# Kernel optimization log

Hardware: AMD Instinct MI355X
Metric: run time of the kernel (lower is better)

## Reference

```python
import jax, jax.numpy as jnp
import numpy as np

N, E, H = 2000, 4096, 256

def setup_inputs() -> dict:
    key = jax.random.key(0)
    ks = jax.random.split(key, 24)
    def rn(k, shape, scale=0.05):
        return jax.random.normal(k, shape, dtype=jnp.float32) * scale
    inp = {
        'x': jax.random.randint(ks[0], (N, 1), 0, 5),
        'pos': rn(ks[1], (N, 3), 1.0),
        'edge_index': jax.random.randint(ks[2], (2, E), 0, N),
        'edge_atr': rn(ks[3], (E, 5), 1.0),
        'emb_table': rn(ks[4], (5, 5), 1.0),
        'lin0_W': rn(ks[5], (H, 8)), 'lin0_b': jnp.zeros((H,), jnp.float32),
        'mlp1_W': rn(ks[6], (128, 5)), 'mlp1_b': jnp.zeros((128,), jnp.float32),
        'mlp2_W': rn(ks[7], (H * H, 128), 0.01), 'mlp2_b': jnp.zeros((H * H,), jnp.float32),
        'conv_b': jnp.zeros((H,), jnp.float32),
        'gru_Wih': rn(ks[8], (3 * H, H)), 'gru_Whh': rn(ks[9], (3 * H, H)),
        'gru_bih': jnp.zeros((3 * H,), jnp.float32), 'gru_bhh': jnp.zeros((3 * H,), jnp.float32),
        'lin1_W': rn(ks[10], (H, 2 * H)), 'lin1_b': jnp.zeros((H,), jnp.float32),
        'lin2_W': rn(ks[11], (242, H)), 'lin2_b': jnp.zeros((242,), jnp.float32),
        'l6_W1': rn(ks[12], (128, 2 * H)), 'l6_b1': jnp.zeros((128,), jnp.float32),
        'bn_g': jnp.ones((128,), jnp.float32), 'bn_b': jnp.zeros((128,), jnp.float32),
        'l6_W2': rn(ks[13], (1, 128)), 'l6_b2': jnp.zeros((1,), jnp.float32),
    }
    return inp

def _gru_step(m, h, Wih, Whh, bih, bhh):
    gi = m @ Wih.T + bih  # [N,3H]
    gh = h @ Whh.T + bhh
    gir, giz, gin = jnp.split(gi, 3, axis=1)
    ghr, ghz, ghn = jnp.split(gh, 3, axis=1)
    r = jax.nn.sigmoid(gir + ghr)
    z = jax.nn.sigmoid(giz + ghz)
    n = jnp.tanh(gin + r * ghn)
    return (1.0 - z) * n + z * h

def reference(x, pos, edge_index, edge_atr, emb_table, lin0_W, lin0_b,
              mlp1_W, mlp1_b, mlp2_W, mlp2_b, conv_b,
              gru_Wih, gru_Whh, gru_bih, gru_bhh,
              lin1_W, lin1_b, lin2_W, lin2_b,
              l6_W1, l6_b1, bn_g, bn_b, l6_W2, l6_b2):
    node_emb = emb_table[x[:, 0]]                      # [N,5]
    in_p = jnp.concatenate([node_emb, pos], axis=1)    # [N,8]
    out = jax.nn.relu(in_p @ lin0_W.T + lin0_b)        # [N,H]
    h = out
    row, col = edge_index[0], edge_index[1]
    # edge-conditioned weights (edge_atr is loop-invariant -> compute once)
    he = jax.nn.relu(edge_atr @ mlp1_W.T + mlp1_b)     # [E,128]
    W_e = (he @ mlp2_W.T + mlp2_b).reshape(E, H, H)    # [E,H,H]
    counts = jnp.clip(jax.ops.segment_sum(jnp.ones((E,), jnp.float32), col, num_segments=N), 1.0)
    for _ in range(3):
        msg = jnp.einsum('eh,eho->eo', out[row], W_e)  # gather + per-edge matmul
        agg = jax.ops.segment_sum(msg, col, num_segments=N) / counts[:, None] + conv_b
        m = jax.nn.relu(agg)
        h = _gru_step(m, h, gru_Wih, gru_Whh, gru_bih, gru_bhh)
        out = h
    out_concat = jnp.concatenate([out[row], out[col]], axis=1)  # [E,2H]
    o1 = jax.nn.relu(out_concat @ lin1_W.T + lin1_b)
    out2 = o1 @ lin2_W.T + lin2_b                       # [E,242]
    # lin6: Linear -> BatchNorm1d (batch stats, training mode) -> ReLU -> Linear
    h1 = out_concat @ l6_W1.T + l6_b1                   # [E,128]
    mu = jnp.mean(h1, axis=0)
    var = jnp.var(h1, axis=0)
    h1n = (h1 - mu) * jax.lax.rsqrt(var + 1e-5) * bn_g + bn_b
    precs = jax.nn.relu(h1n) @ l6_W2.T + l6_b2          # [E,1]
    return (out2, precs)
```

## Files before the change

kernel.cpp:

```cpp
#include <hip/hip_runtime.h>
#include <hip/hip_bf16.h>

constexpr int N_ = 2000;
constexpr int E_ = 4096;
constexpr int H_ = 256;
constexpr int KH_ = 128;
constexpr int NV_ = H_ * KH_;
constexpr int MPAD_ = 2048;
constexpr int NG_ = 768;
constexpr float VSCALE = 64.f;
constexpr float VSCALE_INV = 1.f / 64.f;

typedef short bf16x8 __attribute__((ext_vector_type(8)));
typedef float f32x4  __attribute__((ext_vector_type(4)));
typedef float f32x2  __attribute__((ext_vector_type(2)));

__device__ __forceinline__ float bf_lo(unsigned u) { return __uint_as_float(u << 16); }
__device__ __forceinline__ float bf_hi(unsigned u) { return __uint_as_float(u & 0xffff0000u); }
__device__ __forceinline__ short bfbits(float f) {
    __hip_bfloat16 b = __float2bfloat16(f);
    return *(short*)&b;
}

#define PIPE_WAIT_ENTER(N_OUTST)                                   \
    asm volatile("s_waitcnt vmcnt(" #N_OUTST ")" ::: "memory");    \
    __builtin_amdgcn_s_barrier();                                  \
    asm volatile("" ::: "memory");                                 \
    __builtin_amdgcn_sched_barrier(0);

#define PIPE_EXIT()                                                \
    __builtin_amdgcn_sched_barrier(0);                             \
    asm volatile("" ::: "memory");                                 \
    __builtin_amdgcn_s_barrier();

__global__ void k_lin0(const int* __restrict__ x, const float* __restrict__ pos,
                       const float* __restrict__ emb, const float* __restrict__ W,
                       const float* __restrict__ b, float* __restrict__ out,
                       __hip_bfloat16* __restrict__ Abf) {
    int n = blockIdx.x, t = threadIdx.x;
    if (n >= N_) { Abf[(size_t)n * H_ + t] = __float2bfloat16(0.f); return; }
    __shared__ float in_p[8];
    if (t < 5) in_p[t] = emb[x[n] * 5 + t];
    else if (t < 8) in_p[t] = pos[n * 3 + (t - 5)];
    __syncthreads();
    float acc = b[t];
#pragma unroll
    for (int i = 0; i < 8; i++) acc += in_p[i] * W[t * 8 + i];
    float v = fmaxf(acc, 0.f);
    out[n * H_ + t] = v;
    Abf[(size_t)n * H_ + t] = __float2bfloat16(v);
}

__global__ void k_he(const float* __restrict__ ea, const float* __restrict__ W,
                     const float* __restrict__ b, float* __restrict__ he) {
    int e = blockIdx.x, t = threadIdx.x;
    __shared__ float a[5];
    if (t < 5) a[t] = ea[e * 5 + t];
    __syncthreads();
    float acc = b[t];
#pragma unroll
    for (int i = 0; i < 5; i++) acc += a[i] * W[t * 5 + i];
    he[e * KH_ + t] = fmaxf(acc, 0.f);
}

__global__ void k_counts(const int* __restrict__ ei, float* __restrict__ counts) {
    int e = blockIdx.x * blockDim.x + threadIdx.x;
    if (e < E_) atomicAdd(&counts[ei[E_ + e]], 1.0f);
}

__global__ void k_trans_bt(const float* __restrict__ W, __hip_bfloat16* __restrict__ Bt) {
    __shared__ float tile[32][68];
    int t = threadIdx.x;
    int n0 = blockIdx.x * 64, k0 = blockIdx.y * 32;
#pragma unroll
    for (int i = 0; i < 2; i++) {
        int idx = t + i * 256;
        int kk = idx >> 4, nn = (idx & 15) * 4;
        float4 f = *(const float4*)&W[(size_t)(k0 + kk) * NV_ + n0 + nn];
        *(float4*)&tile[kk][nn] = f;
    }
    __syncthreads();
#pragma unroll
    for (int i = 0; i < 2; i++) {
        int idx = t + i * 256;
        int nn = idx >> 3, k4 = (idx & 7) * 4;
        short4 s;
        s.x = bfbits(tile[k4 + 0][nn]);
        s.y = bfbits(tile[k4 + 1][nn]);
        s.z = bfbits(tile[k4 + 2][nn]);
        s.w = bfbits(tile[k4 + 3][nn]);
        *(short4*)&Bt[(size_t)(n0 + nn) * H_ + k0 + k4] = s;
    }
}

__global__ void k_prep_w(const float* __restrict__ Wih, const float* __restrict__ Whh,
                         const float* __restrict__ lin1W, const float* __restrict__ l6W1,
                         const float* __restrict__ lin2W, const float* __restrict__ b2,
                         __hip_bfloat16* __restrict__ WihB, __hip_bfloat16* __restrict__ WhhB,
                         __hip_bfloat16* __restrict__ Bpk,
                         __hip_bfloat16* __restrict__ lin2Wb, __hip_bfloat16* __restrict__ BtB) {
    int i = blockIdx.x * 256 + threadIdx.x;
    if (i < NG_ * H_) {
        WihB[i] = __float2bfloat16(Wih[i]);
        WhhB[i] = __float2bfloat16(Whh[i]);
    }
    Bpk[i] = __float2bfloat16(i < 256 * 512 ? lin1W[i] : l6W1[i - 256 * 512]);
    if (i < 128 * 2 * H_) {
        int r = i >> 8, k = i & 255;
        lin2Wb[i] = __float2bfloat16(r < 242 ? lin2W[r * H_ + k] : 0.f);
        int o = i >> 8, h = i & 255;
        BtB[o * H_ + h] = __float2bfloat16(b2[h * H_ + o]);
    }
}

__global__ void k_concat(const int* __restrict__ ei, const float* __restrict__ h,
                         __hip_bfloat16* __restrict__ Cbf) {
    int e = blockIdx.x, t = threadIdx.x;
    int r = ei[e], c = ei[E_ + e];
    Cbf[(size_t)e * 512 + t]       = __float2bfloat16(h[(size_t)r * H_ + t]);
    Cbf[(size_t)e * 512 + 256 + t] = __float2bfloat16(h[(size_t)c * H_ + t]);
}

template <int KD, bool RELU, bool OUT_BF16>
__global__ __launch_bounds__(256, 3) void k_gemm_nt(const __hip_bfloat16* __restrict__ A,
                                                    const __hip_bfloat16* __restrict__ Bt,
                                                    float* __restrict__ Cf,
                                                    __hip_bfloat16* __restrict__ Cb,
                                                    const float* __restrict__ bias,
                                                    int ldc, int ncols, int mvalid) {
    __shared__ __align__(16) short As[2][4096];
    __shared__ __align__(16) short Bs[2][4096];
    int t = threadIdx.x;
    int lane = t & 63, wave = t >> 6;
    int wm = wave >> 1, wn = wave & 1;
    int quad = lane >> 4, l16 = lane & 15;
    int row0 = blockIdx.y * 128, col0 = blockIdx.x * 128;

    f32x4 acc[4][4] = {};
    int r_ld = (lane >> 2);
    int koff = (((lane & 3) ^ ((lane >> 3) & 3)) * 8);
    int swz = (l16 >> 1) & 3;
    constexpr int NST = KD / 32;

    auto stage = [&](int buf, int k0) {
#pragma unroll
        for (int c = 0; c < 4; c++) {
            int q = wave * 4 + c;
            int ch = q & 7;
            int r = ch * 16 + r_ld;
            const __hip_bfloat16* gp;
            short* lp;
            if (q < 8) { gp = A  + (size_t)(row0 + r) * KD + k0 + koff; lp = &As[buf][ch * 512]; }
            else       { gp = Bt + (size_t)(col0 + r) * KD + k0 + koff; lp = &Bs[buf][ch * 512]; }
            __builtin_amdgcn_global_load_lds(
                (const __attribute__((address_space(1))) unsigned int*)(uintptr_t)gp,
                (__attribute__((address_space(3))) unsigned int*)(uintptr_t)lp,
                16, 0, 0);
        }
    };

    stage(0, 0);
    for (int kk = 0; kk < NST; kk++) {
        int cur = kk & 1;
        if (kk + 1 < NST) {
            stage(cur ^ 1, (kk + 1) * 32);
            PIPE_WAIT_ENTER(4)
        } else {
            PIPE_WAIT_ENTER(0)
        }
        bf16x8 a[4], b[4];
#pragma unroll
        for (int i = 0; i < 4; i++)
            a[i] = *(const bf16x8*)&As[cur][(wm * 64 + i * 16 + l16) * 32 + ((quad ^ swz) << 3)];
#pragma unroll
        for (int j = 0; j < 4; j++)
            b[j] = *(const bf16x8*)&Bs[cur][(wn * 64 + j * 16 + l16) * 32 + ((quad ^ swz) << 3)];
#pragma unroll
        for (int i = 0; i < 4; i++)
#pragma unroll
            for (int j = 0; j < 4; j++)
                acc[i][j] = __builtin_amdgcn_mfma_f32_16x16x32_bf16(a[i], b[j], acc[i][j], 0, 0, 0);
        PIPE_EXIT()
    }

#pragma unroll
    for (int i = 0; i < 4; i++) {
        int gm0 = row0 + wm * 64 + i * 16 + quad * 4;
#pragma unroll
        for (int r = 0; r < 4; r++) {
            int gm = gm0 + r;
            if (gm < mvalid) {
#pragma unroll
                for (int j = 0; j < 4; j++) {
                    int col = col0 + wn * 64 + l16 + j * 16;
                    if (col < ncols) {
                        float v = acc[i][j][r];
                        if (bias) v += bias[col];
                        if (RELU) v = fmaxf(v, 0.f);
                        if (OUT_BF16) Cb[(size_t)gm * ldc + col] = __float2bfloat16(v);
                        else          Cf[(size_t)gm * ldc + col] = v;
                    }
                }
            }
        }
    }
}

__global__ __launch_bounds__(256, 4) void k_gemm_VP(const __hip_bfloat16* __restrict__ Abf,
                                                    const __hip_bfloat16* __restrict__ Bt,
                                                    const __hip_bfloat16* __restrict__ WhhB,
                                                    const __hip_bfloat16* __restrict__ BtB,
                                                    const float* __restrict__ bhh,
                                                    float* __restrict__ gh,
                                                    float* __restrict__ outb,
                                                    unsigned char* __restrict__ V8) {
    __shared__ __align__(16) short As[2][4096];
    __shared__ __align__(16) short Bs[2][4096];
    int bid = blockIdx.x;
    int t = threadIdx.x;
    int lane = t & 63, wave = t >> 6;
    int wm = wave >> 1, wn = wave & 1;
    int quad = lane >> 4, l16 = lane & 15;
    int r_ld = (lane >> 2);
    int koff = (((lane & 3) ^ ((lane >> 3) & 3)) * 8);
    int swz = (l16 >> 1) & 3;

    if (bid < 128) {
        int pbx = bid & 7, pby = bid >> 3;
        bool ob = (pbx >= 6);
        const __hip_bfloat16* Bp = ob ? BtB : WhhB;
        int col0 = ob ? (pbx - 6) * 128 : pbx * 128;
        int ldc = ob ? H_ : NG_;
        float* C = ob ? outb : gh;
        int row0 = pby * 128;

        f32x4 acc[4][4] = {};
        auto stage = [&](int buf, int k0) {
#pragma unroll
            for (int c = 0; c < 4; c++) {
                int q = wave * 4 + c;
                int ch = q & 7;
                int r = ch * 16 + r_ld;
                const __hip_bfloat16* gp;
                short* lp;
                if (q < 8) { gp = Abf + ((size_t)(row0 + r) << 8) + k0 + koff; lp = &As[buf][ch * 512]; }
                else       { gp = Bp  + ((size_t)(col0 + r) << 8) + k0 + koff; lp = &Bs[buf][ch * 512]; }
                __builtin_amdgcn_global_load_lds(
                    (const __attribute__((address_space(1))) unsigned int*)(uintptr_t)gp,
                    (__attribute__((address_space(3))) unsigned int*)(uintptr_t)lp,
                    16, 0, 0);
            }
        };
        stage(0, 0);
        for (int kk = 0; kk < 8; kk++) {
            int cur = kk & 1;
            if (kk + 1 < 8) {
                stage(cur ^ 1, (kk + 1) * 32);
                PIPE_WAIT_ENTER(4)
            } else {
                PIPE_WAIT_ENTER(0)
            }
            bf16x8 a[4], b[4];
#pragma unroll
            for (int i = 0; i < 4; i++)
                a[i] = *(const bf16x8*)&As[cur][(wm * 64 + i * 16 + l16) * 32 + ((quad ^ swz) << 3)];
#pragma unroll
            for (int j = 0; j < 4; j++)
                b[j] = *(const bf16x8*)&Bs[cur][(wn * 64 + j * 16 + l16) * 32 + ((quad ^ swz) << 3)];
#pragma unroll
            for (int i = 0; i < 4; i++)
#pragma unroll
                for (int j = 0; j < 4; j++)
                    acc[i][j] = __builtin_amdgcn_mfma_f32_16x16x32_bf16(a[i], b[j], acc[i][j], 0, 0, 0);
            PIPE_EXIT()
        }
#pragma unroll
        for (int i = 0; i < 4; i++) {
            int gm0 = row0 + wm * 64 + i * 16 + quad * 4;
#pragma unroll
            for (int r = 0; r < 4; r++) {
                int gm = gm0 + r;
                if (gm < N_) {
#pragma unroll
                    for (int j = 0; j < 4; j++) {
                        int col = col0 + wn * 64 + l16 + j * 16;
                        float v = acc[i][j][r] + (ob ? 0.f : bhh[col]);
                        C[(size_t)gm * ldc + col] = v;
                    }
                }
            }
        }
        return;
    }

    int vb = bid - 128;
    int bx = vb & 255, by = vb >> 8;
    int row0 = by * 128, col0 = bx * 128;
    int obase = bx * 8;
    int kb = (bx >> 5) * 16;
    short* Ps = &As[0][0];

    f32x4 acc[4][4] = {};
    auto stage = [&](int buf, int k0) {
#pragma unroll
        for (int c = 0; c < 4; c++) {
            int q = wave * 4 + c;
            int ch = q & 7;
            const __hip_bfloat16* gp;
            short* lp;
            if (q < 8) {
                gp = Abf + ((size_t)(row0 + ch * 16 + r_ld) << 8) + k0 + koff;
                lp = &As[buf][ch * 512];
            } else {
                int nv = ((obase + ch) & 255) * 128 + kb + r_ld;
                gp = Bt + ((size_t)nv << 8) + k0 + koff;
                lp = &Bs[buf][ch * 512];
            }
            __builtin_amdgcn_global_load_lds(
                (const __attribute__((address_space(1))) unsigned int*)(uintptr_t)gp,
                (__attribute__((address_space(3))) unsigned int*)(uintptr_t)lp,
                16, 0, 0);
        }
    };
    stage(0, 0);
    for (int kk = 0; kk < 8; kk++) {
        int cur = kk & 1;
        if (kk + 1 < 8) {
            stage(cur ^ 1, (kk + 1) * 32);
            PIPE_WAIT_ENTER(4)
        } else {
            PIPE_WAIT_ENTER(0)
        }
        bf16x8 a[4], b[4];
#pragma unroll
        for (int i = 0; i < 4; i++)
            a[i] = *(const bf16x8*)&As[cur][(wm * 64 + i * 16 + l16) * 32 + ((quad ^ swz) << 3)];
#pragma unroll
        for (int j = 0; j < 4; j++)
            b[j] = *(const bf16x8*)&Bs[cur][(wn * 64 + j * 16 + l16) * 32 + ((quad ^ swz) << 3)];
#pragma unroll
        for (int i = 0; i < 4; i++)
#pragma unroll
            for (int j = 0; j < 4; j++)
                acc[i][j] = __builtin_amdgcn_mfma_f32_16x16x32_bf16(a[i], b[j], acc[i][j], 0, 0, 0);
        PIPE_EXIT()
    }

#pragma unroll
    for (int pp = 0; pp < 4; pp++) {
        if (wm == (pp >> 1)) {
#pragma unroll
            for (int ii = 0; ii < 2; ii++) {
                const int i = (pp & 1) * 2 + ii;
                int lr = ii * 16 + quad * 4;
#pragma unroll
                for (int r = 0; r < 4; r++) {
#pragma unroll
                    for (int j = 0; j < 4; j++) {
                        int col = wn * 64 + j * 16 + l16;
                        Ps[(lr + r) * 136 + col] = bfbits(acc[i][j][r] * VSCALE);
                    }
                }
            }
        }
        __syncthreads();
        {
            int row = t >> 3;
            int col = (t & 7) * 16;
            int gm = row0 + pp * 32 + row;
            if (gm < N_) {
                uint4 ua = *(const uint4*)&Ps[row * 136 + col];
                uint4 ub = *(const uint4*)&Ps[row * 136 + col + 8];
                unsigned p0 = __builtin_amdgcn_cvt_pk_fp8_f32(bf_lo(ua.x), bf_hi(ua.x), 0, false);
                p0 = __builtin_amdgcn_cvt_pk_fp8_f32(bf_lo(ua.y), bf_hi(ua.y), p0, true);
                unsigned p1 = __builtin_amdgcn_cvt_pk_fp8_f32(bf_lo(ua.z), bf_hi(ua.z), 0, false);
                p1 = __builtin_amdgcn_cvt_pk_fp8_f32(bf_lo(ua.w), bf_hi(ua.w), p1, true);
                unsigned p2 = __builtin_amdgcn_cvt_pk_fp8_f32(bf_lo(ub.x), bf_hi(ub.x), 0, false);
                p2 = __builtin_amdgcn_cvt_pk_fp8_f32(bf_lo(ub.y), bf_hi(ub.y), p2, true);
                unsigned p3 = __builtin_amdgcn_cvt_pk_fp8_f32(bf_lo(ub.z), bf_hi(ub.z), 0, false);
                p3 = __builtin_amdgcn_cvt_pk_fp8_f32(bf_lo(ub.w), bf_hi(ub.w), p3, true);
                uint4 o4;
                o4.x = p0; o4.y = p1; o4.z = p2; o4.w = p3;
                *(uint4*)(V8 + (size_t)gm * NV_ + col0 + col) = o4;
            }
        }
        __syncthreads();
    }
}

__global__ __launch_bounds__(256, 3) void k_gemm_tail(const __hip_bfloat16* __restrict__ A,
                                                      const __hip_bfloat16* __restrict__ Bpk,
                                                      const float* __restrict__ b1,
                                                      const float* __restrict__ b2,
                                                      __hip_bfloat16* __restrict__ o1bf,
                                                      float* __restrict__ h1) {
    __shared__ __align__(16) short As[2][4096];
    __shared__ __align__(16) short Bs[2][4096];
    int t = threadIdx.x;
    int lane = t & 63, wave = t >> 6;
    int wm = wave >> 1, wn = wave & 1;
    int quad = lane >> 4, l16 = lane & 15;
    int row0 = blockIdx.y * 128, col0 = blockIdx.x * 128;

    f32x4 acc[4][4] = {};
    int r_ld = (lane >> 2);
    int koff = (((lane & 3) ^ ((lane >> 3) & 3)) * 8);
    int swz = (l16 >> 1) & 3;

    auto stage = [&](int buf, int k0) {
#pragma unroll
        for (int c = 0; c < 4; c++) {
            int q = wave * 4 + c;
            int ch = q & 7;
            int r = ch * 16 + r_ld;
            const __hip_bfloat16* gp;
            short* lp;
            if (q < 8) { gp = A   + (size_t)(row0 + r) * 512 + k0 + koff; lp = &As[buf][ch * 512]; }
            else       { gp = Bpk + (size_t)(col0 + r) * 512 + k0 + koff; lp = &Bs[buf][ch * 512]; }
            __builtin_amdgcn_global_load_lds(
                (const __attribute__((address_space(1))) unsigned int*)(uintptr_t)gp,
                (__attribute__((address_space(3))) unsigned int*)(uintptr_t)lp,
                16, 0, 0);
        }
    };

    stage(0, 0);
    for (int kk = 0; kk < 16; kk++) {
        int cur = kk & 1;
        if (kk + 1 < 16) {
            stage(cur ^ 1, (kk + 1) * 32);
            PIPE_WAIT_ENTER(4)
        } else {
            PIPE_WAIT_ENTER(0)
        }
        bf16x8 a[4], b[4];
#pragma unroll
        for (int i = 0; i < 4; i++)
            a[i] = *(const bf16x8*)&As[cur][(wm * 64 + i * 16 + l16) * 32 + ((quad ^ swz) << 3)];
#pragma unroll
        for (int j = 0; j < 4; j++)
            b[j] = *(const bf16x8*)&Bs[cur][(wn * 64 + j * 16 + l16) * 32 + ((quad ^ swz) << 3)];
#pragma unroll
        for (int i = 0; i < 4; i++)
#pragma unroll
            for (int j = 0; j < 4; j++)
                acc[i][j] = __builtin_amdgcn_mfma_f32_16x16x32_bf16(a[i], b[j], acc[i][j], 0, 0, 0);
        PIPE_EXIT()
    }

#pragma unroll
    for (int i = 0; i < 4; i++) {
        int gm0 = row0 + wm * 64 + i * 16 + quad * 4;
#pragma unroll
        for (int r = 0; r < 4; r++) {
            int gm = gm0 + r;
#pragma unroll
            for (int j = 0; j < 4; j++) {
                int col = col0 + wn * 64 + l16 + j * 16;
                float v = acc[i][j][r];
                if (col < 256) {
                    v = fmaxf(v + b1[col], 0.f);
                    o1bf[(size_t)gm * H_ + col] = __float2bfloat16(v);
                } else {
                    h1[(size_t)gm * 128 + (col - 256)] = v + b2[col - 256];
                }
            }
        }
    }
}

__global__ void k_msg(const int* __restrict__ ei, const float* __restrict__ he,
                      const unsigned char* __restrict__ V8, const float* __restrict__ outb,
                      float* __restrict__ agg) {
    int e = blockIdx.x, o = threadIdx.x;
    __shared__ float hs[KH_];
    if (o < KH_) hs[o] = he[e * KH_ + o] * VSCALE_INV;
    __syncthreads();
    int r = ei[e], c = ei[E_ + e];
    float acc = outb[(size_t)r * H_ + o];
    const unsigned char* vbase = V8 + (size_t)r * NV_ + o * 16;
#pragma unroll
    for (int q = 0; q < 8; q++) {
        uint4 u = *(const uint4*)(vbase + (size_t)q * 4096);
        const float* hp = hs + q * 16;
        f32x2 f;
        f = __builtin_amdgcn_cvt_pk_f32_fp8(u.x, false); acc += hp[0]  * f.x + hp[1]  * f.y;
        f = __builtin_amdgcn_cvt_pk_f32_fp8(u.x, true);  acc += hp[2]  * f.x + hp[3]  * f.y;
        f = __builtin_amdgcn_cvt_pk_f32_fp8(u.y, false); acc += hp[4]  * f.x + hp[5]  * f.y;
        f = __builtin_amdgcn_cvt_pk_f32_fp8(u.y, true);  acc += hp[6]  * f.x + hp[7]  * f.y;
        f = __builtin_amdgcn_cvt_pk_f32_fp8(u.z, false); acc += hp[8]  * f.x + hp[9]  * f.y;
        f = __builtin_amdgcn_cvt_pk_f32_fp8(u.z, true);  acc += hp[10] * f.x + hp[11] * f.y;
        f = __builtin_amdgcn_cvt_pk_f32_fp8(u.w, false); acc += hp[12] * f.x + hp[13] * f.y;
        f = __builtin_amdgcn_cvt_pk_f32_fp8(u.w, true);  acc += hp[14] * f.x + hp[15] * f.y;
    }
    atomicAdd(&agg[(size_t)c * H_ + o], acc);
}

__global__ void k_m(float* __restrict__ agg, const float* __restrict__ counts,
                    const float* __restrict__ conv_b, __hip_bfloat16* __restrict__ Mbf) {
    int i = blockIdx.x * blockDim.x + threadIdx.x;
    if (i >= N_ * H_) return;
    int n = i >> 8, o = i & 255;
    float c = fmaxf(counts[n], 1.0f);
    float a = agg[i];
    agg[i] = 0.f;
    Mbf[i] = __float2bfloat16(fmaxf(a / c + conv_b[o], 0.f));
}

__global__ void k_gru_update(const float* __restrict__ gi, const float* __restrict__ gh,
                             float* __restrict__ h, __hip_bfloat16* __restrict__ Abf) {
    int i = blockIdx.x * blockDim.x + threadIdx.x;
    if (i >= N_ * H_) return;
    int n = i >> 8, j = i & 255;
    const float* gip = gi + (size_t)n * NG_;
    const float* ghp = gh + (size_t)n * NG_;
    float r = 1.f / (1.f + expf(-(gip[j] + ghp[j])));
    float z = 1.f / (1.f + expf(-(gip[H_ + j] + ghp[H_ + j])));
    float nn = tanhf(gip[2 * H_ + j] + r * ghp[2 * H_ + j]);
    float hv = (1.f - z) * nn + z * h[i];
    h[i] = hv;
    Abf[i] = __float2bfloat16(hv);
}

__global__ void k_bnstats(const float* __restrict__ h1, float* __restrict__ mu,
                          float* __restrict__ rsig) {
    int j = blockIdx.x, t = threadIdx.x;
    float s = 0.f, ss = 0.f;
    for (int e = t; e < E_; e += 256) {
        float v = h1[(size_t)e * 128 + j];
        s += v;
        ss += v * v;
    }
    __shared__ float rs[256], rss[256];
    rs[t] = s; rss[t] = ss;
    __syncthreads();
    for (int off = 128; off > 0; off >>= 1) {
        if (t < off) { rs[t] += rs[t + off]; rss[t] += rss[t + off]; }
        __syncthreads();
    }
    if (t == 0) {
        float m_ = rs[0] / E_;
        float v_ = rss[0] / E_ - m_ * m_;
        mu[j] = m_;
        rsig[j] = rsqrtf(v_ + 1e-5f);
    }
}

__global__ void k_precs(const float* __restrict__ h1, const float* __restrict__ mu,
                        const float* __restrict__ rsig, const float* __restrict__ g,
                        const float* __restrict__ bb, const float* __restrict__ W2,
                        const float* __restrict__ b2, float* __restrict__ out) {
    int e = blockIdx.x * blockDim.x + threadIdx.x;
    if (e >= E_) return;
    float acc = b2[0];
#pragma unroll 4
    for (int j = 0; j < 128; j++) {
        float v = (h1[(size_t)e * 128 + j] - mu[j]) * rsig[j] * g[j] + bb[j];
        acc += fmaxf(v, 0.f) * W2[j];
    }
    out[(size_t)E_ * 242 + e] = acc;
}

extern "C" void kernel_launch(void* const* d_in, const int* in_sizes, int n_in,
                              void* d_out, int out_size, void* d_ws, size_t ws_size,
                              hipStream_t stream) {
    const int*   x        = (const int*)  d_in[0];
    const float* pos      = (const float*)d_in[1];
    const int*   ei       = (const int*)  d_in[2];
    const float* edge_atr = (const float*)d_in[3];
    const float* emb      = (const float*)d_in[4];
    const float* lin0_W   = (const float*)d_in[5];
    const float* lin0_b   = (const float*)d_in[6];
    const float* mlp1_W   = (const float*)d_in[7];
    const float* mlp1_b   = (const float*)d_in[8];
    const float* mlp2_W   = (const float*)d_in[9];
    const float* mlp2_b   = (const float*)d_in[10];
    const float* conv_b   = (const float*)d_in[11];
    const float* gru_Wih  = (const float*)d_in[12];
    const float* gru_Whh  = (const float*)d_in[13];
    const float* gru_bih  = (const float*)d_in[14];
    const float* gru_bhh  = (const float*)d_in[15];
    const float* lin1_W   = (const float*)d_in[16];
    const float* lin1_b   = (const float*)d_in[17];
    const float* lin2_W   = (const float*)d_in[18];
    const float* lin2_b   = (const float*)d_in[19];
    const float* l6_W1    = (const float*)d_in[20];
    const float* l6_b1    = (const float*)d_in[21];
    const float* bn_g     = (const float*)d_in[22];
    const float* bn_b     = (const float*)d_in[23];
    const float* l6_W2    = (const float*)d_in[24];
    const float* l6_b2    = (const float*)d_in[25];
    float* out = (float*)d_out;

    char* w = (char*)d_ws;
    size_t off = 0;
    auto alloc = [&](size_t bytes) -> void* {
        void* p = w + off;
        off = (off + bytes + 255) & ~(size_t)255;
        return p;
    };
    float* hbuf   = (float*)alloc((size_t)N_ * H_ * 4);
    float* aggm   = (float*)alloc((size_t)N_ * H_ * 4);
    float* outb   = (float*)alloc((size_t)N_ * H_ * 4);
    float* he     = (float*)alloc((size_t)E_ * KH_ * 4);
    float* gi     = (float*)alloc((size_t)N_ * NG_ * 4);
    float* gh     = (float*)alloc((size_t)N_ * NG_ * 4);
    float* h1     = (float*)alloc((size_t)E_ * 128 * 4);
    float* counts = (float*)alloc((size_t)N_ * 4);
    float* mu     = (float*)alloc(128 * 4);
    float* rsig   = (float*)alloc(128 * 4);
    unsigned char* V8      = (unsigned char*)alloc((size_t)N_ * NV_);
    __hip_bfloat16* Abf    = (__hip_bfloat16*)alloc((size_t)MPAD_ * H_ * 2);
    __hip_bfloat16* Mbf    = (__hip_bfloat16*)alloc((size_t)MPAD_ * H_ * 2);
    __hip_bfloat16* Bt     = (__hip_bfloat16*)alloc((size_t)NV_ * H_ * 2);
    __hip_bfloat16* WihB   = (__hip_bfloat16*)alloc((size_t)NG_ * H_ * 2);
    __hip_bfloat16* WhhB   = (__hip_bfloat16*)alloc((size_t)NG_ * H_ * 2);
    __hip_bfloat16* Bpk    = (__hip_bfloat16*)alloc((size_t)384 * 512 * 2);
    __hip_bfloat16* lin2Wb = (__hip_bfloat16*)alloc((size_t)H_ * H_ * 2);
    __hip_bfloat16* BtB    = (__hip_bfloat16*)alloc((size_t)H_ * H_ * 2);
    __hip_bfloat16* Cbf    = (__hip_bfloat16*)alloc((size_t)E_ * 2 * H_ * 2);
    __hip_bfloat16* o1bf   = (__hip_bfloat16*)alloc((size_t)E_ * H_ * 2);

    k_lin0<<<MPAD_, 256, 0, stream>>>(x, pos, emb, lin0_W, lin0_b, hbuf, Abf);
    k_he<<<E_, 128, 0, stream>>>(edge_atr, mlp1_W, mlp1_b, he);
    hipMemsetAsync(counts, 0, (size_t)N_ * 4, stream);
    hipMemsetAsync(aggm, 0, (size_t)N_ * H_ * 4, stream);
    k_counts<<<(E_ + 255) / 256, 256, 0, stream>>>(ei, counts);
    k_trans_bt<<<dim3(NV_ / 64, H_ / 32), 256, 0, stream>>>(mlp2_W, Bt);
    k_prep_w<<<768, 256, 0, stream>>>(gru_Wih, gru_Whh, lin1_W, l6_W1, lin2_W, mlp2_b,
                                      WihB, WhhB, Bpk, lin2Wb, BtB);

    for (int it = 0; it < 3; it++) {
        k_gemm_VP<<<128 + (NV_ / 128) * (MPAD_ / 128), 256, 0, stream>>>(
            Abf, Bt, WhhB, BtB, gru_bhh, gh, outb, V8);
        k_msg<<<E_, 256, 0, stream>>>(ei, he, V8, outb, aggm);
        k_m<<<(N_ * H_ + 255) / 256, 256, 0, stream>>>(aggm, counts, conv_b, Mbf);
        k_gemm_nt<256, false, false><<<dim3(6, MPAD_ / 128), 256, 0, stream>>>(
            Mbf, WihB, gi, nullptr, gru_bih, NG_, NG_, N_);
        k_gru_update<<<(N_ * H_ + 255) / 256, 256, 0, stream>>>(gi, gh, hbuf, Abf);
    }

    k_concat<<<E_, 256, 0, stream>>>(ei, hbuf, Cbf);
    k_gemm_tail<<<dim3(3, E_ / 128), 256, 0, stream>>>(Cbf, Bpk, lin1_b, l6_b1, o1bf, h1);
    k_gemm_nt<256, false, false><<<dim3(2, E_ / 128), 256, 0, stream>>>(
        o1bf, lin2Wb, out, nullptr, lin2_b, 242, 242, E_);
    k_bnstats<<<128, 256, 0, stream>>>(h1, mu, rsig);
    k_precs<<<(E_ + 255) / 256, 256, 0, stream>>>(h1, mu, rsig, bn_g, bn_b, l6_W2, l6_b2, out);
}
```

Before: 458.9 us.

## Fuse mean/relu prologue into GI GEMM and gather-concat into tail GEMM

The separate k_m kernel, which normalized, biased and relu'd the aggregate into bf16, is folded into a new GEMM that reads fp32 aggregates directly and transforms them in registers before writing to LDS. Likewise the concat gather kernel is folded into the tail GEMM, which gathers node rows by edge index. Aggregate zeroing moves into the GRU update. This removes several launches and intermediate buffers per iteration. In exchange, half the waves now do register-staged loads and conversion instead of async global-to-LDS copies, which may weaken the load pipelining.

```diff
diff --git a/kernel.cpp b/kernel.cpp
--- a/kernel.cpp
+++ b/kernel.cpp
@@ -111,14 +111,6 @@
         int o = i >> 8, h = i & 255;
         BtB[o * H_ + h] = __float2bfloat16(b2[h * H_ + o]);
     }
-}
-
-__global__ void k_concat(const int* __restrict__ ei, const float* __restrict__ h,
-                         __hip_bfloat16* __restrict__ Cbf) {
-    int e = blockIdx.x, t = threadIdx.x;
-    int r = ei[e], c = ei[E_ + e];
-    Cbf[(size_t)e * 512 + t]       = __float2bfloat16(h[(size_t)r * H_ + t]);
-    Cbf[(size_t)e * 512 + 256 + t] = __float2bfloat16(h[(size_t)c * H_ + t]);
 }
 
 template <int KD, bool RELU, bool OUT_BF16>
@@ -388,12 +380,140 @@
     }
 }
 
-__global__ __launch_bounds__(256, 3) void k_gemm_tail(const __hip_bfloat16* __restrict__ A,
-                                                      const __hip_bfloat16* __restrict__ Bpk,
-                                                      const float* __restrict__ b1,
-                                                      const float* __restrict__ b2,
-                                                      __hip_bfloat16* __restrict__ o1bf,
-                                                      float* __restrict__ h1) {
+__global__ __launch_bounds__(256, 3) void k_gemm_gi(const float* __restrict__ agg,
+                                                    const float* __restrict__ counts,
+                                                    const float* __restrict__ conv_b,
+                                                    const __hip_bfloat16* __restrict__ WihB,
+                                                    const float* __restrict__ bih,
+                                                    float* __restrict__ gi) {
+    __shared__ __align__(16) short As[2][4096];
+    __shared__ __align__(16) short Bs[2][4096];
+    __shared__ __align__(16) float conv_lds[256];
+    int t = threadIdx.x;
+    int lane = t & 63, wave = t >> 6;
+    int wm = wave >> 1, wn = wave & 1;
+    int quad = lane >> 4, l16 = lane & 15;
+    int row0 = blockIdx.y * 128, col0 = blockIdx.x * 128;
+    int r_ld = (lane >> 2);
+    int koff = (((lane & 3) ^ ((lane >> 3) & 3)) * 8);
+    int swz = (l16 >> 1) & 3;
+    bool arole = (wave < 2);
+
+    conv_lds[t] = conv_b[t];
+    __syncthreads();
+
+    f32x4 acc[4][4] = {};
+    float rcv[4];
+    const float* asrc[4];
+    if (arole) {
+#pragma unroll
+        for (int c = 0; c < 4; c++) {
+            int ch = wave * 4 + c;
+            int row = row0 + ch * 16 + r_ld;
+            int rowc = row < N_ ? row : N_ - 1;
+            rcv[c] = 1.f / fmaxf(counts[rowc], 1.f);
+            asrc[c] = agg + (size_t)rowc * 256;
+        }
+    }
+    float4 R[2][4][2];
+
+    auto loadA = [&](int buf, int k0) {
+#pragma unroll
+        for (int c = 0; c < 4; c++) {
+            R[buf][c][0] = *(const float4*)(asrc[c] + k0 + koff);
+            R[buf][c][1] = *(const float4*)(asrc[c] + k0 + koff + 4);
+        }
+    };
+    auto stageB = [&](int buf, int k0) {
+#pragma unroll
+        for (int c = 0; c < 4; c++) {
+            int ch = (wave * 4 + c) & 7;
+            const __hip_bfloat16* gp = WihB + (size_t)(col0 + ch * 16 + r_ld) * 256 + k0 + koff;
+            short* lp = &Bs[buf][ch * 512];
+            __builtin_amdgcn_global_load_lds(
+                (const __attribute__((address_space(1))) unsigned int*)(uintptr_t)gp,
+                (__attribute__((address_space(3))) unsigned int*)(uintptr_t)lp,
+                16, 0, 0);
+        }
+    };
+    auto writeA = [&](int buf, int k0) {
+        float4 cb0 = *(const float4*)&conv_lds[k0 + koff];
+        float4 cb1 = *(const float4*)&conv_lds[k0 + koff + 4];
+#pragma unroll
+        for (int c = 0; c < 4; c++) {
+            int ch = wave * 4 + c;
+            float rc = rcv[c];
+            float4 a0 = R[buf][c][0], a1 = R[buf][c][1];
+            bf16x8 v;
+            v[0] = bfbits(fmaxf(a0.x * rc + cb0.x, 0.f));
+            v[1] = bfbits(fmaxf(a0.y * rc + cb0.y, 0.f));
+            v[2] = bfbits(fmaxf(a0.z * rc + cb0.z, 0.f));
+            v[3] = bfbits(fmaxf(a0.w * rc + cb0.w, 0.f));
+            v[4] = bfbits(fmaxf(a1.x * rc + cb1.x, 0.f));
+            v[5] = bfbits(fmaxf(a1.y * rc + cb1.y, 0.f));
+            v[6] = bfbits(fmaxf(a1.z * rc + cb1.z, 0.f));
+            v[7] = bfbits(fmaxf(a1.w * rc + cb1.w, 0.f));
+            *(bf16x8*)&As[buf][ch * 512 + lane * 8] = v;
+        }
+    };
+
+    if (arole) loadA(0, 0); else stageB(0, 0);
+#pragma unroll
+    for (int kk = 0; kk < 8; kk++) {
+        const int cur = kk & 1;
+        if (kk + 1 < 8) {
+            if (arole) loadA(cur ^ 1, (kk + 1) * 32);
+            else       stageB(cur ^ 1, (kk + 1) * 32);
+        }
+        if (arole) {
+            writeA(cur, kk * 32);
+            asm volatile("s_waitcnt lgkmcnt(0)" ::: "memory");
+        } else {
+            if (kk + 1 < 8) { asm volatile("s_waitcnt vmcnt(4)" ::: "memory"); }
+            else            { asm volatile("s_waitcnt vmcnt(0)" ::: "memory"); }
+        }
+        __builtin_amdgcn_s_barrier();
+        asm volatile("" ::: "memory");
+        __builtin_amdgcn_sched_barrier(0);
+        bf16x8 a[4], b[4];
+#pragma unroll
+        for (int i = 0; i < 4; i++)
+            a[i] = *(const bf16x8*)&As[cur][(wm * 64 + i * 16 + l16) * 32 + ((quad ^ swz) << 3)];
+#pragma unroll
+        for (int j = 0; j < 4; j++)
+            b[j] = *(const bf16x8*)&Bs[cur][(wn * 64 + j * 16 + l16) * 32 + ((quad ^ swz) << 3)];
+#pragma unroll
+        for (int i = 0; i < 4; i++)
+#pragma unroll
+            for (int j = 0; j < 4; j++)
+                acc[i][j] = __builtin_amdgcn_mfma_f32_16x16x32_bf16(a[i], b[j], acc[i][j], 0, 0, 0);
+        PIPE_EXIT()
+    }
+
+#pragma unroll
+    for (int i = 0; i < 4; i++) {
+        int gm0 = row0 + wm * 64 + i * 16 + quad * 4;
+#pragma unroll
+        for (int r = 0; r < 4; r++) {
+            int gm = gm0 + r;
+            if (gm < N_) {
+#pragma unroll
+                for (int j = 0; j < 4; j++) {
+                    int col = col0 + wn * 64 + l16 + j * 16;
+                    gi[(size_t)gm * NG_ + col] = acc[i][j][r] + bih[col];
+                }
+            }
+        }
+    }
+}
+
+__global__ __launch_bounds__(256, 3) void k_gemm_tail2(const int* __restrict__ ei,
+                                                       const float* __restrict__ h,
+                                                       const __hip_bfloat16* __restrict__ Bpk,
+                                                       const float* __restrict__ b1,
+                                                       const float* __restrict__ b2,
+                                                       __hip_bfloat16* __restrict__ o1bf,
+                                                       float* __restrict__ h1) {
     __shared__ __align__(16) short As[2][4096];
     __shared__ __align__(16) short Bs[2][4096];
     int t = threadIdx.x;
@@ -401,38 +521,77 @@
     int wm = wave >> 1, wn = wave & 1;
     int quad = lane >> 4, l16 = lane & 15;
     int row0 = blockIdx.y * 128, col0 = blockIdx.x * 128;
-
-    f32x4 acc[4][4] = {};
     int r_ld = (lane >> 2);
     int koff = (((lane & 3) ^ ((lane >> 3) & 3)) * 8);
     int swz = (l16 >> 1) & 3;
-
-    auto stage = [&](int buf, int k0) {
-#pragma unroll
-        for (int c = 0; c < 4; c++) {
-            int q = wave * 4 + c;
-            int ch = q & 7;
-            int r = ch * 16 + r_ld;
-            const __hip_bfloat16* gp;
-            short* lp;
-            if (q < 8) { gp = A   + (size_t)(row0 + r) * 512 + k0 + koff; lp = &As[buf][ch * 512]; }
-            else       { gp = Bpk + (size_t)(col0 + r) * 512 + k0 + koff; lp = &Bs[buf][ch * 512]; }
+    bool arole = (wave < 2);
+
+    f32x4 acc[4][4] = {};
+    const float* src0[4];
+    const float* src1[4];
+    if (arole) {
+#pragma unroll
+        for (int c = 0; c < 4; c++) {
+            int ch = wave * 4 + c;
+            int e = row0 + ch * 16 + r_ld;
+            src0[c] = h + (size_t)ei[e] * 256;
+            src1[c] = h + (size_t)ei[E_ + e] * 256;
+        }
+    }
+    float4 R[2][4][2];
+
+    auto loadA = [&](int buf, int k0) {
+        bool hi = (k0 >= 256);
+        int kc = (k0 & 255) + koff;
+#pragma unroll
+        for (int c = 0; c < 4; c++) {
+            const float* s = hi ? src1[c] : src0[c];
+            R[buf][c][0] = *(const float4*)(s + kc);
+            R[buf][c][1] = *(const float4*)(s + kc + 4);
+        }
+    };
+    auto stageB = [&](int buf, int k0) {
+#pragma unroll
+        for (int c = 0; c < 4; c++) {
+            int ch = (wave * 4 + c) & 7;
+            const __hip_bfloat16* gp = Bpk + (size_t)(col0 + ch * 16 + r_ld) * 512 + k0 + koff;
+            short* lp = &Bs[buf][ch * 512];
             __builtin_amdgcn_global_load_lds(
                 (const __attribute__((address_space(1))) unsigned int*)(uintptr_t)gp,
                 (__attribute__((address_space(3))) unsigned int*)(uintptr_t)lp,
                 16, 0, 0);
         }
     };
-
-    stage(0, 0);
+    auto writeA = [&](int buf) {
+#pragma unroll
+        for (int c = 0; c < 4; c++) {
+            int ch = wave * 4 + c;
+            float4 a0 = R[buf][c][0], a1 = R[buf][c][1];
+            bf16x8 v;
+            v[0] = bfbits(a0.x); v[1] = bfbits(a0.y); v[2] = bfbits(a0.z); v[3] = bfbits(a0.w);
+            v[4] = bfbits(a1.x); v[5] = bfbits(a1.y); v[6] = bfbits(a1.z); v[7] = bfbits(a1.w);
+            *(bf16x8*)&As[buf][ch * 512 + lane * 8] = v;
+        }
+    };
+
+    if (arole) loadA(0, 0); else stageB(0, 0);
+#pragma unroll
     for (int kk = 0; kk < 16; kk++) {
-        int cur = kk & 1;
+        const int cur = kk & 1;
         if (kk + 1 < 16) {
-            stage(cur ^ 1, (kk + 1) * 32);
-            PIPE_WAIT_ENTER(4)
+            if (arole) loadA(cur ^ 1, (kk + 1) * 32);
+            else       stageB(cur ^ 1, (kk + 1) * 32);
+        }
+        if (arole) {
+            writeA(cur);
+            asm volatile("s_waitcnt lgkmcnt(0)" ::: "memory");
         } else {
-            PIPE_WAIT_ENTER(0)
-        }
+            if (kk + 1 < 16) { asm volatile("s_waitcnt vmcnt(4)" ::: "memory"); }
+            else             { asm volatile("s_waitcnt vmcnt(0)" ::: "memory"); }
+        }
+        __builtin_amdgcn_s_barrier();
+        asm volatile("" ::: "memory");
+        __builtin_amdgcn_sched_barrier(0);
         bf16x8 a[4], b[4];
 #pragma unroll
         for (int i = 0; i < 4; i++)
@@ -496,19 +655,9 @@
     atomicAdd(&agg[(size_t)c * H_ + o], acc);
 }
 
-__global__ void k_m(float* __restrict__ agg, const float* __restrict__ counts,
-                    const float* __restrict__ conv_b, __hip_bfloat16* __restrict__ Mbf) {
-    int i = blockIdx.x * blockDim.x + threadIdx.x;
-    if (i >= N_ * H_) return;
-    int n = i >> 8, o = i & 255;
-    float c = fmaxf(counts[n], 1.0f);
-    float a = agg[i];
-    agg[i] = 0.f;
-    Mbf[i] = __float2bfloat16(fmaxf(a / c + conv_b[o], 0.f));
-}
-
 __global__ void k_gru_update(const float* __restrict__ gi, const float* __restrict__ gh,
-                             float* __restrict__ h, __hip_bfloat16* __restrict__ Abf) {
+                             float* __restrict__ h, __hip_bfloat16* __restrict__ Abf,
+                             float* __restrict__ agg) {
     int i = blockIdx.x * blockDim.x + threadIdx.x;
     if (i >= N_ * H_) return;
     int n = i >> 8, j = i & 255;
@@ -520,6 +669,7 @@
     float hv = (1.f - z) * nn + z * h[i];
     h[i] = hv;
     Abf[i] = __float2bfloat16(hv);
+    agg[i] = 0.f;
 }
 
 __global__ void k_bnstats(const float* __restrict__ h1, float* __restrict__ mu,
@@ -611,14 +761,12 @@
     float* rsig   = (float*)alloc(128 * 4);
     unsigned char* V8      = (unsigned char*)alloc((size_t)N_ * NV_);
     __hip_bfloat16* Abf    = (__hip_bfloat16*)alloc((size_t)MPAD_ * H_ * 2);
-    __hip_bfloat16* Mbf    = (__hip_bfloat16*)alloc((size_t)MPAD_ * H_ * 2);
     __hip_bfloat16* Bt     = (__hip_bfloat16*)alloc((size_t)NV_ * H_ * 2);
     __hip_bfloat16* WihB   = (__hip_bfloat16*)alloc((size_t)NG_ * H_ * 2);
     __hip_bfloat16* WhhB   = (__hip_bfloat16*)alloc((size_t)NG_ * H_ * 2);
     __hip_bfloat16* Bpk    = (__hip_bfloat16*)alloc((size_t)384 * 512 * 2);
     __hip_bfloat16* lin2Wb = (__hip_bfloat16*)alloc((size_t)H_ * H_ * 2);
     __hip_bfloat16* BtB    = (__hip_bfloat16*)alloc((size_t)H_ * H_ * 2);
-    __hip_bfloat16* Cbf    = (__hip_bfloat16*)alloc((size_t)E_ * 2 * H_ * 2);
     __hip_bfloat16* o1bf   = (__hip_bfloat16*)alloc((size_t)E_ * H_ * 2);
 
     k_lin0<<<MPAD_, 256, 0, stream>>>(x, pos, emb, lin0_W, lin0_b, hbuf, Abf);
@@ -634,14 +782,13 @@
         k_gemm_VP<<<128 + (NV_ / 128) * (MPAD_ / 128), 256, 0, stream>>>(
             Abf, Bt, WhhB, BtB, gru_bhh, gh, outb, V8);
         k_msg<<<E_, 256, 0, stream>>>(ei, he, V8, outb, aggm);
-        k_m<<<(N_ * H_ + 255) / 256, 256, 0, stream>>>(aggm, counts, conv_b, Mbf);
-        k_gemm_nt<256, false, false><<<dim3(6, MPAD_ / 128), 256, 0, stream>>>(
-            Mbf, WihB, gi, nullptr, gru_bih, NG_, NG_, N_);
-        k_gru_update<<<(N_ * H_ + 255) / 256, 256, 0, stream>>>(gi, gh, hbuf, Abf);
-    }
-
-    k_concat<<<E_, 256, 0, stream>>>(ei, hbuf, Cbf);
-    k_gemm_tail<<<dim3(3, E_ / 128), 256, 0, stream>>>(Cbf, Bpk, lin1_b, l6_b1, o1bf, h1);
+        k_gemm_gi<<<dim3(6, MPAD_ / 128), 256, 0, stream>>>(
+            aggm, counts, conv_b, WihB, gru_bih, gi);
+        k_gru_update<<<(N_ * H_ + 255) / 256, 256, 0, stream>>>(gi, gh, hbuf, Abf, aggm);
+    }
+
+    k_gemm_tail2<<<dim3(3, E_ / 128), 256, 0, stream>>>(ei, hbuf, Bpk, lin1_b, l6_b1,
+                                                        o1bf, h1);
     k_gemm_nt<256, false, false><<<dim3(2, E_ / 128), 256, 0, stream>>>(
         o1bf, lin2Wb, out, nullptr, lin2_b, 242, 242, E_);
     k_bnstats<<<128, 256, 0, stream>>>(h1, mu, rsig);
```

Result: slower. 494.3 us (+7.7%).
